# Kernel tuning notes

Measured on AMD Instinct MI355X. Metric: run time of the kernel, lower is better.

The kernel has to match this reference:

```python
import jax, jax.numpy as jnp
import numpy as np

D_IN = 768
D_OUT = 768
NUM_HEADS = 12
HEAD_DIM = D_OUT // NUM_HEADS


def setup_inputs() -> dict:
    key = jax.random.key(0)
    ks = jax.random.split(key, 6)
    s = 0.02
    x = jax.random.normal(ks[0], (2, 4096, D_IN), dtype=jnp.float32)
    w_query = jax.random.normal(ks[1], (D_IN, D_OUT), dtype=jnp.float32) * s
    w_key = jax.random.normal(ks[2], (D_IN, D_OUT), dtype=jnp.float32) * s
    w_value = jax.random.normal(ks[3], (D_IN, D_OUT), dtype=jnp.float32) * s
    w_out = jax.random.normal(ks[4], (D_OUT, D_OUT), dtype=jnp.float32) * s
    b_out = jnp.zeros((D_OUT,), dtype=jnp.float32)
    return {"x": x, "w_query": w_query, "w_key": w_key, "w_value": w_value,
            "w_out": w_out, "b_out": b_out}


def reference(x, w_query, w_key, w_value, w_out, b_out):
    b, n, _ = x.shape
    # projections -> [b, n, h, d]
    q = (x @ w_query).reshape(b, n, NUM_HEADS, HEAD_DIM)
    k = (x @ w_key).reshape(b, n, NUM_HEADS, HEAD_DIM)
    v = (x @ w_value).reshape(b, n, NUM_HEADS, HEAD_DIM)
    # scores [b, h, q, k]
    scores = jnp.einsum('bqhd,bkhd->bhqk', q, k)
    causal = jnp.triu(jnp.ones((n, n), dtype=bool), k=1)  # True above diagonal
    scores = jnp.where(causal, -jnp.inf, scores)
    scale = 1.0 / jnp.sqrt(jnp.asarray(HEAD_DIM, dtype=scores.dtype))
    weights = jax.nn.softmax(scores * scale, axis=-1)
    # dropout p=0.0 -> identity
    ctx = jnp.einsum('bhqk,bkhd->bqhd', weights, v).reshape(b, n, D_OUT)
    return ctx @ w_out + b_out
```

## Files before the change

### kernel.cpp

```cpp
#include <hip/hip_runtime.h>

typedef unsigned short ushort_t;
typedef __bf16 bf16_t;
typedef float floatx4 __attribute__((ext_vector_type(4)));
typedef bf16_t bf16x8 __attribute__((ext_vector_type(8)));
typedef float f32x4 __attribute__((ext_vector_type(4)));
typedef unsigned short u16x4 __attribute__((ext_vector_type(4)));
typedef unsigned int u32x2 __attribute__((ext_vector_type(2)));

#define NTOK 4096
#define NHEAD 12
#define HD 64
#define DMODEL 768
#define NROWS 8192
#define NBH 24

__device__ __forceinline__ ushort_t f2bf(float f) {
  union { float f; unsigned u; } v; v.f = f;
  unsigned u = v.u;
  unsigned r = u + 0x7fffu + ((u >> 16) & 1u);
  return (ushort_t)(r >> 16);
}

__device__ __forceinline__ float bf2f(ushort_t s) {
  union { unsigned u; float f; } v; v.u = (unsigned)s << 16; return v.f;
}

__device__ __forceinline__ void async16(const void* g, void* l) {
  __builtin_amdgcn_global_load_lds(
      (const __attribute__((address_space(1))) void*)g,
      (__attribute__((address_space(3))) void*)l, 16, 0, 0);
}


__global__ __launch_bounds__(256) void transpose_w4(
    const float* __restrict__ s0, const float* __restrict__ s1,
    const float* __restrict__ s2, const float* __restrict__ s3,
    ushort_t* __restrict__ d_qkv, ushort_t* __restrict__ d_o) {
  __shared__ float t[32][33];
  const int m = blockIdx.z;
  const float* src = (m == 0) ? s0 : (m == 1) ? s1 : (m == 2) ? s2 : s3;
  ushort_t* dst = (m < 3) ? (d_qkv + (size_t)m * DMODEL * DMODEL) : d_o;
  const int bi = blockIdx.x, bj = blockIdx.y;
  const int r = threadIdx.x >> 5, c = threadIdx.x & 31;
  for (int p = 0; p < 4; ++p)
    t[r + p * 8][c] = src[(size_t)(bi * 32 + r + p * 8) * DMODEL + bj * 32 + c];
  __syncthreads();
  for (int p = 0; p < 4; ++p)
    dst[(size_t)(bj * 32 + r + p * 8) * DMODEL + bi * 32 + c] = f2bf(t[c][r + p * 8]);
}

__global__ void convert_x(const float* __restrict__ in, ushort_t* __restrict__ out) {
  int idx = blockIdx.x * 256 + threadIdx.x;
  f32x4 v = ((const f32x4*)in)[idx];
  u16x4 o;
  o.x = f2bf(v.x); o.y = f2bf(v.y); o.z = f2bf(v.z); o.w = f2bf(v.w);
  ((u16x4*)out)[idx] = o;
}

__global__ __launch_bounds__(256) void gemm_bt(
    const ushort_t* __restrict__ A, const ushort_t* __restrict__ B, int K, int mode,
    ushort_t* __restrict__ q_ws, ushort_t* __restrict__ k_ws, ushort_t* __restrict__ v_ws,
    float* __restrict__ outF, const float* __restrict__ bias) {
  __shared__ __align__(16) ushort_t a_lds[128 * 32];
  __shared__ __align__(16) ushort_t b_lds[128 * 32];
  const int tid = threadIdx.x;
  const int w = tid >> 6, lane = tid & 63;
  const int quad = lane >> 4, l16 = lane & 15;
  const int wm = w >> 1, wn = w & 1;
  const size_t row0 = (size_t)blockIdx.x * 128;
  const size_t col0 = (size_t)blockIdx.y * 128;

  const int srow = w * 32 + (lane >> 2);
  const int kbyte = (lane & 3) * 16;
  const char* aG = (const char*)(A + (row0 + srow) * (size_t)K) + kbyte;
  const char* bG = (const char*)(B + (col0 + srow) * (size_t)K) + kbyte;
  const size_t rstep = (size_t)16 * K * 2;
  char* aL = (char*)a_lds + (size_t)(w * 2) * 1024;
  char* bL = (char*)b_lds + (size_t)(w * 2) * 1024;

  floatx4 acc[4][4];
  for (int i = 0; i < 4; ++i)
    for (int j = 0; j < 4; ++j) acc[i][j] = (floatx4){0.f, 0.f, 0.f, 0.f};

  const int nk = K / 32;
  for (int kt = 0; kt < nk; ++kt) {
    const size_t koff = (size_t)kt * 64;
    __syncthreads();
    async16(aG + koff, aL);
    async16(aG + koff + rstep, aL + 1024);
    async16(bG + koff, bL);
    async16(bG + koff + rstep, bL + 1024);
    __syncthreads();
    bf16x8 af[4], bfr[4];
    for (int mt = 0; mt < 4; ++mt)
      af[mt] = *(bf16x8*)&a_lds[(wm * 64 + mt * 16 + l16) * 32 + quad * 8];
    for (int nt = 0; nt < 4; ++nt)
      bfr[nt] = *(bf16x8*)&b_lds[(wn * 64 + nt * 16 + l16) * 32 + quad * 8];
    for (int mt = 0; mt < 4; ++mt)
      for (int nt = 0; nt < 4; ++nt)
        acc[mt][nt] = __builtin_amdgcn_mfma_f32_16x16x32_bf16(af[mt], bfr[nt], acc[mt][nt], 0, 0, 0);
  }

  if (mode == 0) {
    const int which = (int)(col0 / DMODEL);
    if (which < 2) {
      ushort_t* dstT = (which == 0) ? q_ws : k_ws;
      const float scale = (which == 0) ? 0.125f * 1.4426950408889634f : 1.0f;
      for (int mt = 0; mt < 4; ++mt) {
        int gr = (int)row0 + wm * 64 + mt * 16 + quad * 4;
        int b = gr >> 12;
        int n0 = gr & 4095;
        for (int nt = 0; nt < 4; ++nt) {
          int gc = (int)col0 + wn * 64 + nt * 16 + l16;
          int cc = gc - which * DMODEL;
          int h = cc >> 6, d = cc & 63;
          size_t base = ((size_t)(b * NHEAD + h) * NTOK + n0) * HD + d;
          for (int r = 0; r < 4; ++r)
            dstT[base + (size_t)r * HD] = f2bf(acc[mt][nt][r] * scale);
        }
      }
    } else {
      for (int mt = 0; mt < 4; ++mt) {
        int gr = (int)row0 + wm * 64 + mt * 16 + quad * 4;
        int b = gr >> 12;
        int n0 = gr & 4095;
        for (int nt = 0; nt < 4; ++nt) {
          int gc = (int)col0 + wn * 64 + nt * 16 + l16;
          int cc = gc - 2 * DMODEL;
          int h = cc >> 6, d = cc & 63;
          u16x4 ov;
          for (int r = 0; r < 4; ++r) ov[r] = f2bf(acc[mt][nt][r]);
          *(u16x4*)&v_ws[((size_t)(b * NHEAD + h) * HD + d) * NTOK + n0] = ov;
        }
      }
    }
  } else {
    for (int mt = 0; mt < 4; ++mt) {
      int gr = (int)row0 + wm * 64 + mt * 16 + quad * 4;
      for (int nt = 0; nt < 4; ++nt) {
        int gc = (int)col0 + wn * 64 + nt * 16 + l16;
        float bv = bias[gc];
        for (int r = 0; r < 4; ++r)
          outF[(size_t)(gr + r) * DMODEL + gc] = acc[mt][nt][r] + bv;
      }
    }
  }
}

__global__ __launch_bounds__(256) void attn5(
    const ushort_t* __restrict__ Qh, const ushort_t* __restrict__ Kh,
    const ushort_t* __restrict__ Vt, ushort_t* __restrict__ o_part,
    float* __restrict__ l_part) {
  __shared__ __align__(16) ushort_t k_lds[2][8 * 512];
  __shared__ __align__(16) ushort_t v_lds[2][8 * 512];
  __shared__ __align__(16) ushort_t q_lds[16 * 512];
  const int tid = threadIdx.x;
  const int w = tid >> 6, lane = tid & 63;
  const int quad = lane >> 4, l16 = lane & 15;
  const int bh = blockIdx.x;
  const int split = blockIdx.z;
  const size_t hbase = (size_t)bh * NTOK * HD;
  const ushort_t* Qb = Qh + hbase;
  const ushort_t* Kb = Kh + hbase;
  const ushort_t* Vb = Vt + hbase;
  const size_t obase = ((size_t)split * NBH + bh) * NTOK * HD;
  const size_t lbase = ((size_t)split * NBH + bh) * NTOK;

  for (int phase = 0; phase < 2; ++phase) {
    const int qt = (phase == 0) ? (int)blockIdx.y : 31 - (int)blockIdx.y;
    const int Q0 = qt * 128;
    const int nkt = 2 * qt + 2;
    const int kt_lo = (split == 0) ? 0 : nkt / 2;
    const int kt_hi = (split == 0) ? nkt / 2 : nkt;
    const int nit = kt_hi - kt_lo;
    __syncthreads();
#pragma unroll
    for (int i = 0; i < 4; ++i) {
      int s = w * 4 + i;
      async16(Qb + (size_t)(Q0 + (s >> 1) * 16 + l16) * HD + (s & 1) * 32 + quad * 8,
              (char*)q_lds + s * 1024);
    }
    {
      const int k0p = kt_lo * 64;
#pragma unroll
      for (int i = 0; i < 2; ++i) {
        int s = w * 2 + i;
        async16(Kb + (size_t)(k0p + (s >> 1) * 16 + l16) * HD + (s & 1) * 32 + quad * 8,
                (char*)k_lds + s * 1024);
        async16(Vb + (size_t)((s >> 1) * 16 + l16) * NTOK + k0p + (s & 1) * 32 + quad * 8,
                (char*)v_lds + s * 1024);
      }
    }
    __asm volatile("s_waitcnt vmcnt(0)" ::: "memory");
    bf16x8 qr[2][2];
#pragma unroll
    for (int qf = 0; qf < 2; ++qf)
#pragma unroll
      for (int hh = 0; hh < 2; ++hh)
        qr[qf][hh] = *(const bf16x8*)((const char*)q_lds + ((w * 4 + qf * 2 + hh) * 1024) + lane * 16);

    floatx4 o[2][4];
    float lp[2] = {0.f, 0.f};
#pragma unroll
    for (int qf = 0; qf < 2; ++qf)
#pragma unroll
      for (int dt = 0; dt < 4; ++dt) o[qf][dt] = (floatx4){0.f, 0.f, 0.f, 0.f};

    const int wq0 = Q0 + w * 32;

    for (int it = 0; it < nit; ++it) {
      const int kt = kt_lo + it;
      const int cur = it & 1;
      __syncthreads();
      if (it + 1 < nit) {
        const int k1 = (kt + 1) * 64;
#pragma unroll
        for (int i = 0; i < 2; ++i) {
          int s = w * 2 + i;
          async16(Kb + (size_t)(k1 + (s >> 1) * 16 + l16) * HD + (s & 1) * 32 + quad * 8,
                  (char*)k_lds + (cur ^ 1) * 8192 + s * 1024);
          async16(Vb + (size_t)((s >> 1) * 16 + l16) * NTOK + k1 + (s & 1) * 32 + quad * 8,
                  (char*)v_lds + (cur ^ 1) * 8192 + s * 1024);
        }
      }
      const int k0 = kt * 64;
      if (k0 > wq0 + 31) continue;
      const char* kb = (const char*)k_lds + cur * 8192;
      const char* vb = (const char*)v_lds + cur * 8192;

      floatx4 st[2][4];
#pragma unroll
      for (int mt = 0; mt < 4; ++mt) {
        bf16x8 kf0 = *(const bf16x8*)(kb + (mt * 2 + 0) * 1024 + lane * 16);
        bf16x8 kf1 = *(const bf16x8*)(kb + (mt * 2 + 1) * 1024 + lane * 16);
#pragma unroll
        for (int qf = 0; qf < 2; ++qf) {
          floatx4 z = (floatx4){0.f, 0.f, 0.f, 0.f};
          z = __builtin_amdgcn_mfma_f32_16x16x32_bf16(kf0, qr[qf][0], z, 0, 0, 0);
          z = __builtin_amdgcn_mfma_f32_16x16x32_bf16(kf1, qr[qf][1], z, 0, 0, 0);
          st[qf][mt] = z;
        }
      }
      const bool need_mask = (k0 + 63 > wq0);
#pragma unroll
      for (int qf = 0; qf < 2; ++qf) {
        const int qg = wq0 + qf * 16 + l16;
        float sum = 0.f;
#pragma unroll
        for (int mt = 0; mt < 4; ++mt) {
          float p[4];
#pragma unroll
          for (int r = 0; r < 4; ++r) {
            float e = __builtin_exp2f(st[qf][mt][r]);
            if (need_mask && (k0 + mt * 16 + quad * 4 + r > qg)) e = 0.f;
            p[r] = e;
            sum += e;
          }
          union { float f; unsigned u; } c0, c1, c2, c3;
          c0.f = p[0]; c1.f = p[1]; c2.f = p[2]; c3.f = p[3];
          u32x2 pk;
          pk.x = __builtin_amdgcn_perm(c1.u, c0.u, 0x07060302u);
          pk.y = __builtin_amdgcn_perm(c3.u, c2.u, 0x07060302u);
          char* dst = (char*)q_lds + ((w * 4 + qf * 2 + (mt >> 1)) * 1024)
                      + ((((mt & 1) * 2 + (quad >> 1)) * 16 + l16) * 16) + (quad & 1) * 8;
          *(u32x2*)dst = pk;
        }
        lp[qf] += sum;
      }
      __asm volatile("s_waitcnt lgkmcnt(0)" ::: "memory");
      bf16x8 pf[2][2];
#pragma unroll
      for (int qf = 0; qf < 2; ++qf)
#pragma unroll
        for (int hh = 0; hh < 2; ++hh)
          pf[qf][hh] = *(const bf16x8*)((const char*)q_lds + ((w * 4 + qf * 2 + hh) * 1024) + lane * 16);
#pragma unroll
      for (int dt = 0; dt < 4; ++dt) {
        bf16x8 vf0 = *(const bf16x8*)(vb + (dt * 2 + 0) * 1024 + lane * 16);
        bf16x8 vf1 = *(const bf16x8*)(vb + (dt * 2 + 1) * 1024 + lane * 16);
#pragma unroll
        for (int qf = 0; qf < 2; ++qf) {
          o[qf][dt] = __builtin_amdgcn_mfma_f32_16x16x32_bf16(pf[qf][0], vf0, o[qf][dt], 0, 0, 0);
          o[qf][dt] = __builtin_amdgcn_mfma_f32_16x16x32_bf16(pf[qf][1], vf1, o[qf][dt], 0, 0, 0);
        }
      }
    }

#pragma unroll
    for (int qf = 0; qf < 2; ++qf) {
      float lf = lp[qf];
      lf += __shfl_xor(lf, 16);
      lf += __shfl_xor(lf, 32);
#pragma unroll
      for (int r = 0; r < 4; ++r) {
        float lq = __shfl(lf, quad * 4 + r);
        int qg = wq0 + qf * 16 + quad * 4 + r;
        size_t base = obase + (size_t)qg * HD;
#pragma unroll
        for (int dt = 0; dt < 4; ++dt)
          o_part[base + dt * 16 + l16] = f2bf(o[qf][dt][r]);
        if (l16 == 0) l_part[lbase + qg] = lq;
      }
    }
  }
}

__global__ __launch_bounds__(256) void combine(
    const ushort_t* __restrict__ o_part, const float* __restrict__ l_part,
    ushort_t* __restrict__ ctx) {
  const int row = blockIdx.x * 16 + (threadIdx.x >> 4);
  const int d = (threadIdx.x & 15) * 4;
  const int bh = row >> 12, n = row & 4095;
  const int b = bh / NHEAD, h = bh % NHEAD;
  const size_t i0 = (size_t)row * HD + d;
  const size_t i1 = i0 + (size_t)NBH * NTOK * HD;
  u16x4 a = *(const u16x4*)&o_part[i0];
  u16x4 c = *(const u16x4*)&o_part[i1];
  float inv = 1.0f / (l_part[row] + l_part[row + NBH * NTOK]);
  u16x4 ov;
#pragma unroll
  for (int j = 0; j < 4; ++j) ov[j] = f2bf((bf2f(a[j]) + bf2f(c[j])) * inv);
  *(u16x4*)&ctx[((size_t)b * NTOK + n) * DMODEL + h * HD + d] = ov;
}

extern "C" void kernel_launch(void* const* d_in, const int* in_sizes, int n_in,
                              void* d_out, int out_size, void* d_ws, size_t ws_size,
                              hipStream_t stream) {
  const float* x  = (const float*)d_in[0];
  const float* wq = (const float*)d_in[1];
  const float* wk = (const float*)d_in[2];
  const float* wv = (const float*)d_in[3];
  const float* wo = (const float*)d_in[4];
  const float* bo = (const float*)d_in[5];
  float* out = (float*)d_out;

  ushort_t* ws = (ushort_t*)d_ws;
  ushort_t* wqkvT = ws;
  ushort_t* woutT = wqkvT + 2304 * 768;
  ushort_t* xbf   = woutT + 768 * 768;
  ushort_t* qh    = xbf + (size_t)NROWS * DMODEL;
  ushort_t* kh    = qh + (size_t)NBH * NTOK * HD;
  ushort_t* vt    = kh + (size_t)NBH * NTOK * HD;
  ushort_t* opart = vt + (size_t)NBH * NTOK * HD;
  float*    lpart = (float*)(opart + (size_t)2 * NBH * NTOK * HD);

  transpose_w4<<<dim3(24, 24, 4), 256, 0, stream>>>(wq, wk, wv, wo, wqkvT, woutT);
  convert_x<<<6144, 256, 0, stream>>>(x, xbf);

  gemm_bt<<<dim3(64, 18), 256, 0, stream>>>(xbf, wqkvT, DMODEL, 0,
                                            qh, kh, vt, nullptr, nullptr);
  attn5<<<dim3(24, 16, 2), 256, 0, stream>>>(qh, kh, vt, opart, lpart);
  combine<<<(NBH * NTOK) / 16, 256, 0, stream>>>(opart, lpart, xbf );
  gemm_bt<<<dim3(64, 6), 256, 0, stream>>>(xbf, woutT, DMODEL, 1,
                                           nullptr, nullptr, nullptr, out, bo);
}
```

Measured before the change: 282.6 us.

## Fuse split-combine into output GEMM, widen attention waves, pack V stores

Removes the separate combine kernel. The output-projection GEMM (mode 2) now loads both split partials and the row sums directly, normalises them, and writes the result to LDS as its A tile. The attention kernel goes from 4 waves to 2 waves per block, with each wave handling 64 query rows and the score computation split into two halves to limit register pressure. The V-transpose store in the QKV GEMM exchanges halves between lanes so it can write 16-byte vectors. The fused path replaces async loads with synchronous global loads inside the K loop and redoes the combine work once per column block, and halving the threads per attention block changes how much latency the kernel can hide.

```diff
diff --git a/kernel.cpp b/kernel.cpp
--- a/kernel.cpp
+++ b/kernel.cpp
@@ -6,6 +6,7 @@
 typedef bf16_t bf16x8 __attribute__((ext_vector_type(8)));
 typedef float f32x4 __attribute__((ext_vector_type(4)));
 typedef unsigned short u16x4 __attribute__((ext_vector_type(4)));
+typedef unsigned short u16x8 __attribute__((ext_vector_type(8)));
 typedef unsigned int u32x2 __attribute__((ext_vector_type(2)));
 
 #define NTOK 4096
@@ -61,7 +62,8 @@
 __global__ __launch_bounds__(256) void gemm_bt(
     const ushort_t* __restrict__ A, const ushort_t* __restrict__ B, int K, int mode,
     ushort_t* __restrict__ q_ws, ushort_t* __restrict__ k_ws, ushort_t* __restrict__ v_ws,
-    float* __restrict__ outF, const float* __restrict__ bias) {
+    float* __restrict__ outF, const float* __restrict__ bias,
+    const ushort_t* __restrict__ opart, const float* __restrict__ lpart) {
   __shared__ __align__(16) ushort_t a_lds[128 * 32];
   __shared__ __align__(16) ushort_t b_lds[128 * 32];
   const int tid = threadIdx.x;
@@ -87,8 +89,28 @@
   for (int kt = 0; kt < nk; ++kt) {
     const size_t koff = (size_t)kt * 64;
     __syncthreads();
-    async16(aG + koff, aL);
-    async16(aG + koff + rstep, aL + 1024);
+    if (mode == 2) {
+      const int col = kt * 32 + (lane & 3) * 8;
+      const int h = col >> 6, dd = col & 63;
+#pragma unroll
+      for (int sl = 0; sl < 2; ++sl) {
+        int row = (int)row0 + srow + sl * 16;
+        int b = row >> 12, n = row & 4095;
+        int bh = b * NHEAD + h;
+        size_t i0 = ((size_t)bh * NTOK + n) * HD + dd;
+        size_t i1 = i0 + (size_t)NBH * NTOK * HD;
+        u16x8 a = *(const u16x8*)&opart[i0];
+        u16x8 c = *(const u16x8*)&opart[i1];
+        float inv = 1.0f / (lpart[(size_t)bh * NTOK + n] + lpart[(size_t)(NBH + bh) * NTOK + n]);
+        u16x8 o;
+#pragma unroll
+        for (int j = 0; j < 8; ++j) o[j] = f2bf((bf2f(a[j]) + bf2f(c[j])) * inv);
+        *(u16x8*)(aL + sl * 1024 + (size_t)lane * 16) = o;
+      }
+    } else {
+      async16(aG + koff, aL);
+      async16(aG + koff + rstep, aL + 1024);
+    }
     async16(bG + koff, bL);
     async16(bG + koff + rstep, bL + 1024);
     __syncthreads();
@@ -131,7 +153,15 @@
           int h = cc >> 6, d = cc & 63;
           u16x4 ov;
           for (int r = 0; r < 4; ++r) ov[r] = f2bf(acc[mt][nt][r]);
-          *(u16x4*)&v_ws[((size_t)(b * NHEAD + h) * HD + d) * NTOK + n0] = ov;
+          unsigned d0 = ((unsigned*)&ov)[0], d1 = ((unsigned*)&ov)[1];
+          unsigned p0 = (unsigned)__shfl_xor((int)d0, 16);
+          unsigned p1 = (unsigned)__shfl_xor((int)d1, 16);
+          if (!(quad & 1)) {
+            u16x8 pk;
+            ((unsigned*)&pk)[0] = d0; ((unsigned*)&pk)[1] = d1;
+            ((unsigned*)&pk)[2] = p0; ((unsigned*)&pk)[3] = p1;
+            *(u16x8*)&v_ws[((size_t)(b * NHEAD + h) * HD + d) * NTOK + n0] = pk;
+          }
         }
       }
     }
@@ -148,7 +178,7 @@
   }
 }
 
-__global__ __launch_bounds__(256) void attn5(
+__global__ __launch_bounds__(128, 2) void attn6(
     const ushort_t* __restrict__ Qh, const ushort_t* __restrict__ Kh,
     const ushort_t* __restrict__ Vt, ushort_t* __restrict__ o_part,
     float* __restrict__ l_part) {
@@ -176,16 +206,16 @@
     const int nit = kt_hi - kt_lo;
     __syncthreads();
 #pragma unroll
-    for (int i = 0; i < 4; ++i) {
-      int s = w * 4 + i;
-      async16(Qb + (size_t)(Q0 + (s >> 1) * 16 + l16) * HD + (s & 1) * 32 + quad * 8,
+    for (int i = 0; i < 8; ++i) {
+      int s = w * 8 + i;
+      async16(Qb + (size_t)(Q0 + w * 64 + (i >> 1) * 16 + l16) * HD + (i & 1) * 32 + quad * 8,
               (char*)q_lds + s * 1024);
     }
     {
       const int k0p = kt_lo * 64;
 #pragma unroll
-      for (int i = 0; i < 2; ++i) {
-        int s = w * 2 + i;
+      for (int i = 0; i < 4; ++i) {
+        int s = w * 4 + i;
         async16(Kb + (size_t)(k0p + (s >> 1) * 16 + l16) * HD + (s & 1) * 32 + quad * 8,
                 (char*)k_lds + s * 1024);
         async16(Vb + (size_t)((s >> 1) * 16 + l16) * NTOK + k0p + (s & 1) * 32 + quad * 8,
@@ -193,21 +223,21 @@
       }
     }
     __asm volatile("s_waitcnt vmcnt(0)" ::: "memory");
-    bf16x8 qr[2][2];
-#pragma unroll
-    for (int qf = 0; qf < 2; ++qf)
+    bf16x8 qr[4][2];
+#pragma unroll
+    for (int qf = 0; qf < 4; ++qf)
 #pragma unroll
       for (int hh = 0; hh < 2; ++hh)
-        qr[qf][hh] = *(const bf16x8*)((const char*)q_lds + ((w * 4 + qf * 2 + hh) * 1024) + lane * 16);
-
-    floatx4 o[2][4];
-    float lp[2] = {0.f, 0.f};
-#pragma unroll
-    for (int qf = 0; qf < 2; ++qf)
+        qr[qf][hh] = *(const bf16x8*)((const char*)q_lds + ((w * 8 + qf * 2 + hh) * 1024) + lane * 16);
+
+    floatx4 o[4][4];
+    float lp[4] = {0.f, 0.f, 0.f, 0.f};
+#pragma unroll
+    for (int qf = 0; qf < 4; ++qf)
 #pragma unroll
       for (int dt = 0; dt < 4; ++dt) o[qf][dt] = (floatx4){0.f, 0.f, 0.f, 0.f};
 
-    const int wq0 = Q0 + w * 32;
+    const int wq0 = Q0 + w * 64;
 
     for (int it = 0; it < nit; ++it) {
       const int kt = kt_lo + it;
@@ -216,8 +246,8 @@
       if (it + 1 < nit) {
         const int k1 = (kt + 1) * 64;
 #pragma unroll
-        for (int i = 0; i < 2; ++i) {
-          int s = w * 2 + i;
+        for (int i = 0; i < 4; ++i) {
+          int s = w * 4 + i;
           async16(Kb + (size_t)(k1 + (s >> 1) * 16 + l16) * HD + (s & 1) * 32 + quad * 8,
                   (char*)k_lds + (cur ^ 1) * 8192 + s * 1024);
           async16(Vb + (size_t)((s >> 1) * 16 + l16) * NTOK + k1 + (s & 1) * 32 + quad * 8,
@@ -225,62 +255,67 @@
         }
       }
       const int k0 = kt * 64;
-      if (k0 > wq0 + 31) continue;
+      if (k0 > wq0 + 63) continue;
       const char* kb = (const char*)k_lds + cur * 8192;
       const char* vb = (const char*)v_lds + cur * 8192;
-
-      floatx4 st[2][4];
-#pragma unroll
-      for (int mt = 0; mt < 4; ++mt) {
-        bf16x8 kf0 = *(const bf16x8*)(kb + (mt * 2 + 0) * 1024 + lane * 16);
-        bf16x8 kf1 = *(const bf16x8*)(kb + (mt * 2 + 1) * 1024 + lane * 16);
-#pragma unroll
-        for (int qf = 0; qf < 2; ++qf) {
-          floatx4 z = (floatx4){0.f, 0.f, 0.f, 0.f};
-          z = __builtin_amdgcn_mfma_f32_16x16x32_bf16(kf0, qr[qf][0], z, 0, 0, 0);
-          z = __builtin_amdgcn_mfma_f32_16x16x32_bf16(kf1, qr[qf][1], z, 0, 0, 0);
-          st[qf][mt] = z;
-        }
-      }
       const bool need_mask = (k0 + 63 > wq0);
-#pragma unroll
-      for (int qf = 0; qf < 2; ++qf) {
-        const int qg = wq0 + qf * 16 + l16;
-        float sum = 0.f;
-#pragma unroll
-        for (int mt = 0; mt < 4; ++mt) {
-          float p[4];
-#pragma unroll
-          for (int r = 0; r < 4; ++r) {
-            float e = __builtin_exp2f(st[qf][mt][r]);
-            if (need_mask && (k0 + mt * 16 + quad * 4 + r > qg)) e = 0.f;
-            p[r] = e;
-            sum += e;
+
+#pragma unroll
+      for (int half = 0; half < 2; ++half) {
+        floatx4 st[4][2];
+#pragma unroll
+        for (int m2 = 0; m2 < 2; ++m2) {
+          const int mt = half * 2 + m2;
+          bf16x8 kf0 = *(const bf16x8*)(kb + (mt * 2 + 0) * 1024 + lane * 16);
+          bf16x8 kf1 = *(const bf16x8*)(kb + (mt * 2 + 1) * 1024 + lane * 16);
+#pragma unroll
+          for (int qf = 0; qf < 4; ++qf) {
+            floatx4 z = (floatx4){0.f, 0.f, 0.f, 0.f};
+            z = __builtin_amdgcn_mfma_f32_16x16x32_bf16(kf0, qr[qf][0], z, 0, 0, 0);
+            z = __builtin_amdgcn_mfma_f32_16x16x32_bf16(kf1, qr[qf][1], z, 0, 0, 0);
+            st[qf][m2] = z;
           }
-          union { float f; unsigned u; } c0, c1, c2, c3;
-          c0.f = p[0]; c1.f = p[1]; c2.f = p[2]; c3.f = p[3];
-          u32x2 pk;
-          pk.x = __builtin_amdgcn_perm(c1.u, c0.u, 0x07060302u);
-          pk.y = __builtin_amdgcn_perm(c3.u, c2.u, 0x07060302u);
-          char* dst = (char*)q_lds + ((w * 4 + qf * 2 + (mt >> 1)) * 1024)
-                      + ((((mt & 1) * 2 + (quad >> 1)) * 16 + l16) * 16) + (quad & 1) * 8;
-          *(u32x2*)dst = pk;
-        }
-        lp[qf] += sum;
+        }
+#pragma unroll
+        for (int qf = 0; qf < 4; ++qf) {
+          const int qg = wq0 + qf * 16 + l16;
+          float sum = 0.f;
+#pragma unroll
+          for (int m2 = 0; m2 < 2; ++m2) {
+            const int mt = half * 2 + m2;
+            float p[4];
+#pragma unroll
+            for (int r = 0; r < 4; ++r) {
+              float e = __builtin_exp2f(st[qf][m2][r]);
+              if (need_mask && (k0 + mt * 16 + quad * 4 + r > qg)) e = 0.f;
+              p[r] = e;
+              sum += e;
+            }
+            union { float f; unsigned u; } c0, c1, c2, c3;
+            c0.f = p[0]; c1.f = p[1]; c2.f = p[2]; c3.f = p[3];
+            u32x2 pk;
+            pk.x = __builtin_amdgcn_perm(c1.u, c0.u, 0x07060302u);
+            pk.y = __builtin_amdgcn_perm(c3.u, c2.u, 0x07060302u);
+            char* dst = (char*)q_lds + ((w * 8 + qf * 2 + (mt >> 1)) * 1024)
+                        + ((((mt & 1) * 2 + (quad >> 1)) * 16 + l16) * 16) + (quad & 1) * 8;
+            *(u32x2*)dst = pk;
+          }
+          lp[qf] += sum;
+        }
       }
       __asm volatile("s_waitcnt lgkmcnt(0)" ::: "memory");
-      bf16x8 pf[2][2];
-#pragma unroll
-      for (int qf = 0; qf < 2; ++qf)
+      bf16x8 pf[4][2];
+#pragma unroll
+      for (int qf = 0; qf < 4; ++qf)
 #pragma unroll
         for (int hh = 0; hh < 2; ++hh)
-          pf[qf][hh] = *(const bf16x8*)((const char*)q_lds + ((w * 4 + qf * 2 + hh) * 1024) + lane * 16);
+          pf[qf][hh] = *(const bf16x8*)((const char*)q_lds + ((w * 8 + qf * 2 + hh) * 1024) + lane * 16);
 #pragma unroll
       for (int dt = 0; dt < 4; ++dt) {
         bf16x8 vf0 = *(const bf16x8*)(vb + (dt * 2 + 0) * 1024 + lane * 16);
         bf16x8 vf1 = *(const bf16x8*)(vb + (dt * 2 + 1) * 1024 + lane * 16);
 #pragma unroll
-        for (int qf = 0; qf < 2; ++qf) {
+        for (int qf = 0; qf < 4; ++qf) {
           o[qf][dt] = __builtin_amdgcn_mfma_f32_16x16x32_bf16(pf[qf][0], vf0, o[qf][dt], 0, 0, 0);
           o[qf][dt] = __builtin_amdgcn_mfma_f32_16x16x32_bf16(pf[qf][1], vf1, o[qf][dt], 0, 0, 0);
         }
@@ -288,7 +323,7 @@
     }
 
 #pragma unroll
-    for (int qf = 0; qf < 2; ++qf) {
+    for (int qf = 0; qf < 4; ++qf) {
       float lf = lp[qf];
       lf += __shfl_xor(lf, 16);
       lf += __shfl_xor(lf, 32);
@@ -304,24 +339,6 @@
       }
     }
   }
-}
-
-__global__ __launch_bounds__(256) void combine(
-    const ushort_t* __restrict__ o_part, const float* __restrict__ l_part,
-    ushort_t* __restrict__ ctx) {
-  const int row = blockIdx.x * 16 + (threadIdx.x >> 4);
-  const int d = (threadIdx.x & 15) * 4;
-  const int bh = row >> 12, n = row & 4095;
-  const int b = bh / NHEAD, h = bh % NHEAD;
-  const size_t i0 = (size_t)row * HD + d;
-  const size_t i1 = i0 + (size_t)NBH * NTOK * HD;
-  u16x4 a = *(const u16x4*)&o_part[i0];
-  u16x4 c = *(const u16x4*)&o_part[i1];
-  float inv = 1.0f / (l_part[row] + l_part[row + NBH * NTOK]);
-  u16x4 ov;
-#pragma unroll
-  for (int j = 0; j < 4; ++j) ov[j] = f2bf((bf2f(a[j]) + bf2f(c[j])) * inv);
-  *(u16x4*)&ctx[((size_t)b * NTOK + n) * DMODEL + h * HD + d] = ov;
 }
 
 extern "C" void kernel_launch(void* const* d_in, const int* in_sizes, int n_in,
@@ -349,9 +366,8 @@
   convert_x<<<6144, 256, 0, stream>>>(x, xbf);
 
   gemm_bt<<<dim3(64, 18), 256, 0, stream>>>(xbf, wqkvT, DMODEL, 0,
-                                            qh, kh, vt, nullptr, nullptr);
-  attn5<<<dim3(24, 16, 2), 256, 0, stream>>>(qh, kh, vt, opart, lpart);
-  combine<<<(NBH * NTOK) / 16, 256, 0, stream>>>(opart, lpart, xbf );
-  gemm_bt<<<dim3(64, 6), 256, 0, stream>>>(xbf, woutT, DMODEL, 1,
-                                           nullptr, nullptr, nullptr, out, bo);
-}
+                                            qh, kh, vt, nullptr, nullptr, nullptr, nullptr);
+  attn6<<<dim3(24, 16, 2), 128, 0, stream>>>(qh, kh, vt, opart, lpart);
+  gemm_bt<<<dim3(64, 6), 256, 0, stream>>>(opart, woutT, DMODEL, 2,
+                                           nullptr, nullptr, nullptr, out, bo, opart, lpart);
+}
```

After: 313.0 us. 1.11x slower.
